# Kernel optimization log

Measured on AMD Instinct MI355X. Metric: run time of the kernel, lower is better.

The kernel has to match this reference:

```python
import jax, jax.numpy as jnp
import numpy as np

E = 768       # embedding_dim
H = 12        # num_heads
ID = 768      # inter_dim
HD = ID // H  # head_dim = 64
DHX = HD // 2  # 32
DHY = HD - DHX  # 32
HP, WP = 16, 16
P = HP * WP
BASE = 10000.0
SCALE = HD ** -0.5


def rot_half(x):
    x1 = x[..., 0::2]
    x2 = x[..., 1::2]
    return jnp.stack([-x2, x1], axis=-1).reshape(x.shape)


def apply_rope(x, cos, sin):
    cos = jnp.repeat(cos, 2, axis=-1)
    sin = jnp.repeat(sin, 2, axis=-1)
    return x * cos + rot_half(x) * sin


def rope_cache(L, dim, base):
    inv_freq = 1.0 / base ** (jnp.arange(0, dim, 2, dtype=jnp.float32) / dim)
    t = jnp.arange(L, dtype=jnp.float32)
    freqs = t[:, None] * inv_freq[None, :]  # [L, dim//2]
    return jnp.cos(freqs), jnp.sin(freqs)


def _rope_tables():
    yy, xx = jnp.meshgrid(jnp.arange(HP), jnp.arange(WP), indexing='ij')
    py = yy.reshape(P)
    px = xx.reshape(P)
    cos_x, sin_x = rope_cache(WP, DHX, BASE)
    cos_y, sin_y = rope_cache(HP, DHY, BASE)
    # gather per-patch tables, shape (1,1,P,1,D/2)
    cx = cos_x[px].reshape(1, 1, P, 1, DHX // 2)
    sx = sin_x[px].reshape(1, 1, P, 1, DHX // 2)
    cy = cos_y[py].reshape(1, 1, P, 1, DHY // 2)
    sy = sin_y[py].reshape(1, 1, P, 1, DHY // 2)
    return cx, sx, cy, sy


def setup_inputs() -> dict:
    key = jax.random.key(0)
    ks = jax.random.split(key, 8)
    B, T = 8, 16
    x = jax.random.normal(ks[0], (B, T, P, E), dtype=jnp.float32)
    s = 0.02
    return {
        'x': x,
        'Wq': jax.random.normal(ks[1], (E, ID), dtype=jnp.float32) * s,
        'bq': jnp.zeros((ID,), dtype=jnp.float32),
        'Wk': jax.random.normal(ks[2], (E, ID), dtype=jnp.float32) * s,
        'bk': jnp.zeros((ID,), dtype=jnp.float32),
        'Wv': jax.random.normal(ks[3], (E, ID), dtype=jnp.float32) * s,
        'bv': jnp.zeros((ID,), dtype=jnp.float32),
        'Wo': jax.random.normal(ks[4], (ID, E), dtype=jnp.float32) * s,
    }


def reference(x, Wq, bq, Wk, bk, Wv, bv, Wo):
    B, T, Pn, _ = x.shape
    q = (x @ Wq + bq).reshape(B, T, Pn, H, HD)
    k = (x @ Wk + bk).reshape(B, T, Pn, H, HD)
    v = (x @ Wv + bv).reshape(B, T, Pn, H, HD)

    cx, sx, cy, sy = _rope_tables()
    qx, qy = q[..., :DHX], q[..., DHX:]
    kx, ky = k[..., :DHX], k[..., DHX:]
    q = jnp.concatenate([apply_rope(qx, cx, sx), apply_rope(qy, cy, sy)], axis=-1)
    k = jnp.concatenate([apply_rope(kx, cx, sx), apply_rope(ky, cy, sy)], axis=-1)

    scores = jnp.einsum('btihd,btjhd->bthij', q, k) * SCALE
    probs = jax.nn.softmax(scores, axis=-1)
    y = jnp.einsum('bthij,btjhd->btihd', probs, v).reshape(B, T, Pn, ID)
    return y @ Wo
```

## Files before the change

kernel.cpp:

```cpp
#include <hip/hip_runtime.h>
#include <hip/hip_bf16.h>
#include <cstdint>
#include <cstddef>

typedef __bf16 bf16;
typedef __bf16 bf16x8 __attribute__((ext_vector_type(8)));
typedef __bf16 bf16x4 __attribute__((ext_vector_type(4)));
typedef float  f32x4  __attribute__((ext_vector_type(4)));

#define MFMA_BF16(a,b,c) __builtin_amdgcn_mfma_f32_16x16x32_bf16((a),(b),(c),0,0,0)

#define BB 8
#define TT 16
#define PP 256
#define EE 768
#define HH 12
#define HDD 64
#define NQKV 2304
#define MROWS 32768

__device__ __forceinline__ void gld_lds16(const bf16* g, bf16* l) {
  __builtin_amdgcn_global_load_lds((const __attribute__((address_space(1))) void*)g,
                                   (__attribute__((address_space(3))) void*)l, 16, 0, 0);
}

__global__ __launch_bounds__(256) void k_cvt_x(const float* __restrict__ x,
                                               bf16* __restrict__ xb) {
  const int64_t i = (int64_t)blockIdx.x * 256 + threadIdx.x;
  const float4* src = (const float4*)x;
  float4 a = src[i * 2];
  float4 b = src[i * 2 + 1];
  bf16x8 o;
  o[0] = (bf16)a.x; o[1] = (bf16)a.y; o[2] = (bf16)a.z; o[3] = (bf16)a.w;
  o[4] = (bf16)b.x; o[5] = (bf16)b.y; o[6] = (bf16)b.z; o[7] = (bf16)b.w;
  *(bf16x8*)(xb + i * 8) = o;
}

__global__ __launch_bounds__(256) void k_wt(const float* __restrict__ Wq,
                                            const float* __restrict__ Wk,
                                            const float* __restrict__ Wv,
                                            const float* __restrict__ Wo,
                                            bf16* __restrict__ wt) {
  __shared__ float tile[32][33];
  const int n0 = blockIdx.x * 32;
  const int k0 = blockIdx.y * 32;
  const float* W;
  int nc;
  if (n0 < 768)        { W = Wq; nc = n0; }
  else if (n0 < 1536)  { W = Wk; nc = n0 - 768; }
  else if (n0 < 2304)  { W = Wv; nc = n0 - 1536; }
  else                 { W = Wo; nc = n0 - 2304; }
  const int tx = threadIdx.x & 31, ty = threadIdx.x >> 5;
  for (int r = ty; r < 32; r += 8)
    tile[r][tx] = W[(int64_t)(k0 + r) * 768 + nc + tx];
  __syncthreads();
  for (int r = ty; r < 32; r += 8)
    wt[(int64_t)(n0 + r) * 768 + k0 + tx] = (bf16)tile[tx][r];
}

__global__ __launch_bounds__(256) void k_qkv(const bf16* __restrict__ xb,
                                             const bf16* __restrict__ wt,
                                             const float* __restrict__ bq,
                                             const float* __restrict__ bk,
                                             const float* __restrict__ bv,
                                             bf16* __restrict__ qb,
                                             bf16* __restrict__ kb,
                                             bf16* __restrict__ vt) {
  __shared__ __align__(16) bf16 As[128 * 32];
  __shared__ __align__(16) bf16 Bs[128 * 32];
  const int tid  = threadIdx.x;
  const int w    = tid >> 6, lane = tid & 63, quad = lane >> 4, l16 = lane & 15;
  const int bid = blockIdx.x;
  const int xcd = bid & 7;
  const int loc = bid >> 3;
  const int m0  = (xcd * 32 + loc / 18) * 128;
  const int n0  = (loc % 18) * 128;
  const int arow = tid >> 2, aseg = (tid & 3) * 8;
  const bf16* Ag = xb + (int64_t)(m0 + arow) * 768 + aseg;
  const bf16* Bg = wt + (int64_t)(n0 + arow) * 768 + aseg;
  bf16* AsW0 = As + (size_t)w * 512;
  bf16* AsW1 = As + 2048 + (size_t)w * 512;
  bf16* BsW0 = Bs + (size_t)w * 512;
  bf16* BsW1 = Bs + 2048 + (size_t)w * 512;
  const int mb = (w & 1) * 64, nb = (w >> 1) * 64;
  f32x4 acc[4][4] = {};
  for (int kt = 0; kt < 24; ++kt) {
    const int k0 = kt * 32;
    gld_lds16(Ag + k0, AsW0);
    gld_lds16(Ag + 64 * 768 + k0, AsW1);
    gld_lds16(Bg + k0, BsW0);
    gld_lds16(Bg + 64 * 768 + k0, BsW1);
    __syncthreads();
    bf16x8 af[4], bfr[4];
#pragma unroll
    for (int i = 0; i < 4; ++i)
      af[i] = *(const bf16x8*)&As[(mb + i * 16 + l16) * 32 + quad * 8];
#pragma unroll
    for (int i = 0; i < 4; ++i)
      bfr[i] = *(const bf16x8*)&Bs[(nb + i * 16 + l16) * 32 + quad * 8];
#pragma unroll
    for (int mi = 0; mi < 4; ++mi)
#pragma unroll
      for (int ni = 0; ni < 4; ++ni)
        acc[mi][ni] = MFMA_BF16(af[mi], bfr[ni], acc[mi][ni]);
    __syncthreads();
  }
  const int sec = n0 / 768;
  const int nl0 = (n0 % 768) + nb;
  const float* bias_p = (sec == 0) ? bq : (sec == 1) ? bk : bv;
  if (sec == 2) {
#pragma unroll
    for (int ni = 0; ni < 4; ++ni) {
      const int ng = nl0 + ni * 16 + l16;
      const int h = ng >> 6, hd = ng & 63;
      const float bias = bias_p[ng];
#pragma unroll
      for (int mi = 0; mi < 4; ++mi) {
        const int rb = m0 + mb + mi * 16 + quad * 4;
        const int bt = rb >> 8, p = rb & 255;
        bf16x4 pk;
#pragma unroll
        for (int r = 0; r < 4; ++r) pk[r] = (bf16)(acc[mi][ni][r] + bias);
        *(bf16x4*)&vt[((int64_t)(bt * 12 + h) * 64 + hd) * 256 + p] = pk;
      }
    }
  } else {
    bf16* dst = (sec == 0) ? qb : kb;
    const float L2C = 0.83048202372184058696f;
#pragma unroll
    for (int ni = 0; ni < 4; ++ni) {
      const int ng = nl0 + ni * 16 + l16;
      const int h = ng >> 6, hd = ng & 63;
      const float bias = bias_p[ng];
      const int j = (hd & 31) >> 1;
      const float invf = exp2f(-(float)j * L2C);
      const bool odd = (hd & 1);
      const bool isx = (hd < 32);
#pragma unroll
      for (int mi = 0; mi < 4; ++mi) {
        const int rb = m0 + mb + mi * 16 + quad * 4;
        const int bt = rb >> 8;
        const int pb = rb & 255;
#pragma unroll
        for (int r = 0; r < 4; ++r) {
          const int p = pb + r;
          float v = acc[mi][ni][r] + bias;
          float pv = __shfl_xor(v, 1, 64);
          const int pos = isx ? (p & 15) : (p >> 4);
          float sn, cs;
          __sincosf((float)pos * invf, &sn, &cs);
          float o = odd ? (v * cs + pv * sn) : (v * cs - pv * sn);
          dst[((int64_t)(bt * 12 + h) * 256 + p) * 64 + hd] = (bf16)o;
        }
      }
    }
  }
}

__global__ __launch_bounds__(256) void k_attn(bf16* qy,
                                              const bf16* __restrict__ kb,
                                              const bf16* __restrict__ vt) {
  __shared__ __align__(16) bf16 plds[4][16 * 264];
  const int tid = threadIdx.x;
  const int w = tid >> 6, lane = tid & 63, quad = lane >> 4, l16 = lane & 15;
  const int64_t base = (int64_t)blockIdx.x * 16384;
  bf16* Q = qy + base;
  const bf16* K = kb + base;
  const bf16* V = vt + base;
  bf16* pl = plds[w];
  for (int s = 0; s < 4; ++s) {
    const int r0 = w * 64 + s * 16;
    bf16x8 qf0 = *(const bf16x8*)&Q[(r0 + l16) * 64 + quad * 8];
    bf16x8 qf1 = *(const bf16x8*)&Q[(r0 + l16) * 64 + 32 + quad * 8];
    f32x4 sacc[16] = {};
#pragma unroll
    for (int ct = 0; ct < 16; ++ct) {
      bf16x8 kf0 = *(const bf16x8*)&K[(ct * 16 + l16) * 64 + quad * 8];
      bf16x8 kf1 = *(const bf16x8*)&K[(ct * 16 + l16) * 64 + 32 + quad * 8];
      sacc[ct] = MFMA_BF16(qf0, kf0, sacc[ct]);
      sacc[ct] = MFMA_BF16(qf1, kf1, sacc[ct]);
    }
    float mx[4] = {-3e38f, -3e38f, -3e38f, -3e38f};
#pragma unroll
    for (int ct = 0; ct < 16; ++ct)
#pragma unroll
      for (int r = 0; r < 4; ++r) mx[r] = fmaxf(mx[r], sacc[ct][r]);
#pragma unroll
    for (int d = 1; d < 16; d <<= 1)
#pragma unroll
      for (int r = 0; r < 4; ++r) mx[r] = fmaxf(mx[r], __shfl_xor(mx[r], d, 64));
    float sm[4] = {0.f, 0.f, 0.f, 0.f};
#pragma unroll
    for (int ct = 0; ct < 16; ++ct)
#pragma unroll
      for (int r = 0; r < 4; ++r) {
        float e = __expf((sacc[ct][r] - mx[r]) * 0.125f);
        sacc[ct][r] = e;
        sm[r] += e;
      }
#pragma unroll
    for (int d = 1; d < 16; d <<= 1)
#pragma unroll
      for (int r = 0; r < 4; ++r) sm[r] += __shfl_xor(sm[r], d, 64);
#pragma unroll
    for (int ct = 0; ct < 16; ++ct)
#pragma unroll
      for (int r = 0; r < 4; ++r)
        pl[(quad * 4 + r) * 264 + ct * 16 + l16] = (bf16)sacc[ct][r];
    __syncthreads();
    f32x4 oacc[4] = {};
#pragma unroll
    for (int kc = 0; kc < 8; ++kc) {
      bf16x8 pf = *(const bf16x8*)&pl[l16 * 264 + kc * 32 + quad * 8];
#pragma unroll
      for (int nt = 0; nt < 4; ++nt) {
        bf16x8 vf = *(const bf16x8*)&V[(nt * 16 + l16) * 256 + kc * 32 + quad * 8];
        oacc[nt] = MFMA_BF16(pf, vf, oacc[nt]);
      }
    }
    float inv[4];
#pragma unroll
    for (int r = 0; r < 4; ++r) inv[r] = 1.0f / sm[r];
#pragma unroll
    for (int nt = 0; nt < 4; ++nt)
#pragma unroll
      for (int r = 0; r < 4; ++r)
        Q[(r0 + quad * 4 + r) * 64 + nt * 16 + l16] = (bf16)(oacc[nt][r] * inv[r]);
    __syncthreads();
  }
}

__global__ __launch_bounds__(256) void k_out(const bf16* __restrict__ yb,
                                             const bf16* __restrict__ wt,
                                             float* __restrict__ out) {
  __shared__ __align__(16) bf16 As[128 * 32];
  __shared__ __align__(16) bf16 Bs[128 * 32];
  const int tid = threadIdx.x;
  const int w = tid >> 6, lane = tid & 63, quad = lane >> 4, l16 = lane & 15;
  const int bid = blockIdx.x;
  const int xcd = bid & 7;
  const int loc = bid >> 3;
  const int m0  = (xcd * 32 + loc / 6) * 128;
  const int n0  = (loc % 6) * 128;
  const int bt = m0 >> 8, p0 = m0 & 255;
  const int arow = tid >> 2, aseg = (tid & 3) * 8;
  const bf16* Bg = wt + (int64_t)(2304 + n0 + arow) * 768 + aseg;
  bf16* AsW0 = As + (size_t)w * 512;
  bf16* AsW1 = As + 2048 + (size_t)w * 512;
  bf16* BsW0 = Bs + (size_t)w * 512;
  bf16* BsW1 = Bs + 2048 + (size_t)w * 512;
  const int mb = (w & 1) * 64, nb = (w >> 1) * 64;
  f32x4 acc[4][4] = {};
  for (int kt = 0; kt < 24; ++kt) {
    const int h = kt >> 1, hd0 = (kt & 1) * 32;
    const bf16* Ag = yb + ((int64_t)(bt * 12 + h) * 256 + p0 + arow) * 64 + hd0 + aseg;
    gld_lds16(Ag, AsW0);
    gld_lds16(Ag + 64 * 64, AsW1);
    gld_lds16(Bg + kt * 32, BsW0);
    gld_lds16(Bg + 64 * 768 + kt * 32, BsW1);
    __syncthreads();
    bf16x8 af[4], bfr[4];
#pragma unroll
    for (int i = 0; i < 4; ++i)
      af[i] = *(const bf16x8*)&As[(mb + i * 16 + l16) * 32 + quad * 8];
#pragma unroll
    for (int i = 0; i < 4; ++i)
      bfr[i] = *(const bf16x8*)&Bs[(nb + i * 16 + l16) * 32 + quad * 8];
#pragma unroll
    for (int mi = 0; mi < 4; ++mi)
#pragma unroll
      for (int ni = 0; ni < 4; ++ni)
        acc[mi][ni] = MFMA_BF16(af[mi], bfr[ni], acc[mi][ni]);
    __syncthreads();
  }
#pragma unroll
  for (int mi = 0; mi < 4; ++mi)
#pragma unroll
    for (int ni = 0; ni < 4; ++ni) {
      const int rg = m0 + mb + mi * 16 + quad * 4;
      const int cg = n0 + nb + ni * 16 + l16;
#pragma unroll
      for (int r = 0; r < 4; ++r)
        out[(int64_t)(rg + r) * 768 + cg] = acc[mi][ni][r];
    }
}

extern "C" void kernel_launch(void* const* d_in, const int* in_sizes, int n_in,
                              void* d_out, int out_size, void* d_ws, size_t ws_size,
                              hipStream_t stream) {
  const float* x  = (const float*)d_in[0];
  const float* Wq = (const float*)d_in[1];
  const float* bq = (const float*)d_in[2];
  const float* Wk = (const float*)d_in[3];
  const float* bk = (const float*)d_in[4];
  const float* Wv = (const float*)d_in[5];
  const float* bv = (const float*)d_in[6];
  const float* Wo = (const float*)d_in[7];
  float* out = (float*)d_out;

  uint8_t* ws = (uint8_t*)d_ws;
  const size_t SZ = (size_t)25165824 * 2;
  bf16* qy = (bf16*)ws;
  bf16* kb = (bf16*)(ws + SZ);
  bf16* vt = (bf16*)(ws + 2 * SZ);
  bf16* wt = (bf16*)(ws + 3 * SZ);
  bf16* xb = (bf16*)d_out;

  k_cvt_x<<<12288, 256, 0, stream>>>(x, xb);
  k_wt<<<dim3(96, 24), 256, 0, stream>>>(Wq, Wk, Wv, Wo, wt);
  k_qkv<<<4608, 256, 0, stream>>>(xb, wt, bq, bk, bv, qy, kb, vt);
  k_attn<<<1536, 256, 0, stream>>>(qy, kb, vt);
  k_out<<<1536, 256, 0, stream>>>(qy, wt, out);
}
```

Before: 557.7 us.

## Restructure QKV GEMM into 256x256 tiles with double-buffered swizzled LDS

The QKV projection GEMM moves from 128x128 tiles with 4 waves and K-step 32 to 256x256 tiles with 8 waves and K-step 64. LDS is double-buffered so the next K-slice loads while the current one is computed, and an XOR swizzle on the LDS layout avoids bank conflicts. Each wave accumulates 128x64 outputs, and the MFMA bursts are wrapped in setprio. This is meant to raise arithmetic intensity and hide global-load latency, at the cost of 128KB of dynamic LDS per block, more registers and fewer, larger blocks.

```diff
diff --git a/kernel.cpp b/kernel.cpp
--- a/kernel.cpp
+++ b/kernel.cpp
@@ -58,65 +58,89 @@
     wt[(int64_t)(n0 + r) * 768 + k0 + tx] = (bf16)tile[tx][r];
 }
 
-__global__ __launch_bounds__(256) void k_qkv(const bf16* __restrict__ xb,
-                                             const bf16* __restrict__ wt,
-                                             const float* __restrict__ bq,
-                                             const float* __restrict__ bk,
-                                             const float* __restrict__ bv,
-                                             bf16* __restrict__ qb,
-                                             bf16* __restrict__ kb,
-                                             bf16* __restrict__ vt) {
-  __shared__ __align__(16) bf16 As[128 * 32];
-  __shared__ __align__(16) bf16 Bs[128 * 32];
-  const int tid  = threadIdx.x;
-  const int w    = tid >> 6, lane = tid & 63, quad = lane >> 4, l16 = lane & 15;
+__global__ __launch_bounds__(512, 2) void k_qkv(const bf16* __restrict__ xb,
+                                                const bf16* __restrict__ wt,
+                                                const float* __restrict__ bq,
+                                                const float* __restrict__ bk,
+                                                const float* __restrict__ bv,
+                                                bf16* __restrict__ qb,
+                                                bf16* __restrict__ kb,
+                                                bf16* __restrict__ vt) {
+  extern __shared__ char smem_raw[];
+  bf16* smem = (bf16*)smem_raw;
+  const int tid = threadIdx.x;
+  const int w = tid >> 6, lane = tid & 63, quad = lane >> 4, l16 = lane & 15;
+  const int wr = w >> 2, wc = w & 3;
+  const int kap = l16 & 7;
   const int bid = blockIdx.x;
   const int xcd = bid & 7;
   const int loc = bid >> 3;
-  const int m0  = (xcd * 32 + loc / 18) * 128;
-  const int n0  = (loc % 18) * 128;
-  const int arow = tid >> 2, aseg = (tid & 3) * 8;
-  const bf16* Ag = xb + (int64_t)(m0 + arow) * 768 + aseg;
-  const bf16* Bg = wt + (int64_t)(n0 + arow) * 768 + aseg;
-  bf16* AsW0 = As + (size_t)w * 512;
-  bf16* AsW1 = As + 2048 + (size_t)w * 512;
-  bf16* BsW0 = Bs + (size_t)w * 512;
-  bf16* BsW1 = Bs + 2048 + (size_t)w * 512;
-  const int mb = (w & 1) * 64, nb = (w >> 1) * 64;
-  f32x4 acc[4][4] = {};
-  for (int kt = 0; kt < 24; ++kt) {
-    const int k0 = kt * 32;
-    gld_lds16(Ag + k0, AsW0);
-    gld_lds16(Ag + 64 * 768 + k0, AsW1);
-    gld_lds16(Bg + k0, BsW0);
-    gld_lds16(Bg + 64 * 768 + k0, BsW1);
-    __syncthreads();
-    bf16x8 af[4], bfr[4];
-#pragma unroll
-    for (int i = 0; i < 4; ++i)
-      af[i] = *(const bf16x8*)&As[(mb + i * 16 + l16) * 32 + quad * 8];
-#pragma unroll
-    for (int i = 0; i < 4; ++i)
-      bfr[i] = *(const bf16x8*)&Bs[(nb + i * 16 + l16) * 32 + quad * 8];
-#pragma unroll
-    for (int mi = 0; mi < 4; ++mi)
-#pragma unroll
-      for (int ni = 0; ni < 4; ++ni)
-        acc[mi][ni] = MFMA_BF16(af[mi], bfr[ni], acc[mi][ni]);
+  const int m0  = (xcd * 16 + loc / 9) * 256;
+  const int n0  = (loc % 9) * 256;
+  const int srow = w * 8 + (lane >> 3);
+  const int cgo  = ((lane & 7) ^ ((lane >> 3) & 7)) * 8;
+  const bf16* Ag = xb + (int64_t)(m0 + srow) * 768 + cgo;
+  const bf16* Bg = wt + (int64_t)(n0 + srow) * 768 + cgo;
+
+  auto stage = [&](int kt, int p) {
+    bf16* LA = smem + p * 32768 + w * 512;
+    bf16* LB = LA + 16384;
+    const bf16* GA = Ag + kt * 64;
+    const bf16* GB = Bg + kt * 64;
+#pragma unroll
+    for (int rd = 0; rd < 4; ++rd) {
+      gld_lds16(GA + rd * 49152, LA + rd * 4096);
+      gld_lds16(GB + rd * 49152, LB + rd * 4096);
+    }
+  };
+
+  f32x4 acc[8][4] = {};
+  stage(0, 0);
+  __syncthreads();
+  for (int t = 0; t < 12; ++t) {
+    if (t < 11) stage(t + 1, (t + 1) & 1);
+    __builtin_amdgcn_sched_barrier(0);
+    const bf16* A = smem + (t & 1) * 32768;
+    const bf16* B = A + 16384;
+    bf16x8 bfr[4][2];
+#pragma unroll
+    for (int ni = 0; ni < 4; ++ni)
+#pragma unroll
+      for (int kk = 0; kk < 2; ++kk)
+        bfr[ni][kk] = *(const bf16x8*)&B[(wc * 64 + ni * 16 + l16) * 64 +
+                                         (((kk * 4 + quad) ^ kap) * 8)];
+#pragma unroll
+    for (int mh = 0; mh < 2; ++mh) {
+      bf16x8 afr[4][2];
+#pragma unroll
+      for (int mi = 0; mi < 4; ++mi)
+#pragma unroll
+        for (int kk = 0; kk < 2; ++kk)
+          afr[mi][kk] = *(const bf16x8*)&A[(wr * 128 + mh * 64 + mi * 16 + l16) * 64 +
+                                           (((kk * 4 + quad) ^ kap) * 8)];
+      __builtin_amdgcn_s_setprio(1);
+#pragma unroll
+      for (int mi = 0; mi < 4; ++mi)
+#pragma unroll
+        for (int ni = 0; ni < 4; ++ni)
+#pragma unroll
+          for (int kk = 0; kk < 2; ++kk)
+            acc[mh * 4 + mi][ni] = MFMA_BF16(afr[mi][kk], bfr[ni][kk], acc[mh * 4 + mi][ni]);
+      __builtin_amdgcn_s_setprio(0);
+    }
     __syncthreads();
   }
   const int sec = n0 / 768;
-  const int nl0 = (n0 % 768) + nb;
   const float* bias_p = (sec == 0) ? bq : (sec == 1) ? bk : bv;
   if (sec == 2) {
 #pragma unroll
     for (int ni = 0; ni < 4; ++ni) {
-      const int ng = nl0 + ni * 16 + l16;
+      const int ng = (n0 % 768) + wc * 64 + ni * 16 + l16;
       const int h = ng >> 6, hd = ng & 63;
       const float bias = bias_p[ng];
 #pragma unroll
-      for (int mi = 0; mi < 4; ++mi) {
-        const int rb = m0 + mb + mi * 16 + quad * 4;
+      for (int mi = 0; mi < 8; ++mi) {
+        const int rb = m0 + wr * 128 + mi * 16 + quad * 4;
         const int bt = rb >> 8, p = rb & 255;
         bf16x4 pk;
 #pragma unroll
@@ -129,7 +153,7 @@
     const float L2C = 0.83048202372184058696f;
 #pragma unroll
     for (int ni = 0; ni < 4; ++ni) {
-      const int ng = nl0 + ni * 16 + l16;
+      const int ng = (n0 % 768) + wc * 64 + ni * 16 + l16;
       const int h = ng >> 6, hd = ng & 63;
       const float bias = bias_p[ng];
       const int j = (hd & 31) >> 1;
@@ -137,8 +161,8 @@
       const bool odd = (hd & 1);
       const bool isx = (hd < 32);
 #pragma unroll
-      for (int mi = 0; mi < 4; ++mi) {
-        const int rb = m0 + mb + mi * 16 + quad * 4;
+      for (int mi = 0; mi < 8; ++mi) {
+        const int rb = m0 + wr * 128 + mi * 16 + quad * 4;
         const int bt = rb >> 8;
         const int pb = rb & 255;
 #pragma unroll
@@ -306,9 +330,16 @@
   bf16* wt = (bf16*)(ws + 3 * SZ);
   bf16* xb = (bf16*)d_out;
 
+  static int attr_set = 0;
+  if (!attr_set) {
+    (void)hipFuncSetAttribute((const void*)k_qkv,
+                              hipFuncAttributeMaxDynamicSharedMemorySize, 131072);
+    attr_set = 1;
+  }
+
   k_cvt_x<<<12288, 256, 0, stream>>>(x, xb);
   k_wt<<<dim3(96, 24), 256, 0, stream>>>(Wq, Wk, Wv, Wo, wt);
-  k_qkv<<<4608, 256, 0, stream>>>(xb, wt, bq, bk, bv, qy, kb, vt);
+  k_qkv<<<1152, 512, 131072, stream>>>(xb, wt, bq, bk, bv, qy, kb, vt);
   k_attn<<<1536, 256, 0, stream>>>(qy, kb, vt);
   k_out<<<1536, 256, 0, stream>>>(qy, wt, out);
 }
```

Measured after the change: 526.5 us. -5.6%, faster.
